# Kernel tuning notes

Hardware: AMD Instinct MI355X
Metric: run time of the kernel (lower is better)

The kernel has to match this reference:

```python
import jax, jax.numpy as jnp
import numpy as np

# Model dims
B, T, E, H = 2, 2048, 512, 8
HEAD_DIM = E // H            # 64
NUM_SCALES = 4               # Gauss-Laguerre quadrature nodes
NUM_PRF = 16                 # positive random features per scale
POLY_DIM = 16                # degree-2 TensorSketch dim
EPS = 1e-5
CHUNK = 128                  # chunk size for exact chunked causal linear attention


def setup_inputs() -> dict:
    key = jax.random.key(0)
    ks = jax.random.split(key, 10)
    x = jax.random.normal(ks[0], (B, T, E), jnp.float32)
    sc = 1.0 / np.sqrt(E)  # xavier-ish scale for square projections
    Wq = jax.random.normal(ks[1], (E, E), jnp.float32) * sc
    Wk = jax.random.normal(ks[2], (E, E), jnp.float32) * sc
    Wv = jax.random.normal(ks[3], (E, E), jnp.float32) * sc
    Wo = jax.random.normal(ks[4], (E, E), jnp.float32) * sc
    # FAVOR+ gaussian projections, one block per quadrature scale
    projections = jax.random.normal(ks[5], (NUM_SCALES, NUM_PRF, HEAD_DIM), jnp.float32)
    # Gauss-Laguerre nodes/weights for 1/(C - 2 q.k) = int_0^inf exp(-t(C - 2 q.k)) dt
    nodes, weights = np.polynomial.laguerre.laggauss(NUM_SCALES)
    coef = weights * np.exp(nodes) * np.exp(-nodes * EPS)
    scales = jnp.asarray(np.stack([nodes, coef], axis=1), jnp.float32)  # [S, 2] = (t_s, c_s)
    # degree-2 TensorSketch (count-sketch hashes + rademacher signs)
    sketch_h = jax.random.randint(ks[6], (2, HEAD_DIM), 0, POLY_DIM)
    sketch_s = (jax.random.randint(ks[7], (2, HEAD_DIM), 0, 2) * 2 - 1).astype(jnp.float32)
    return dict(x=x, Wq=Wq, Wk=Wk, Wv=Wv, Wo=Wo, projections=projections,
                scales=scales, sketch_h=sketch_h, sketch_s=sketch_s)


def _features(u, projections, scales, sketch_h, sketch_s):
    """Multi-scale FAVOR+ x TensorSketch feature map for the spherical YAT kernel.

    u: [B,T,H,d], unit-normalized along d. Returns [B,T,H, P*S*m].
    Phi(q).Phi(k) ~= (q.k)^2 / (||q-k||^2 + eps).
    """
    t = scales[:, 0]  # quadrature nodes t_s
    c = scales[:, 1]  # quadrature coeffs w_s e^{t_s} e^{-t_s eps}
    S, m, d = projections.shape
    z = jnp.einsum('smd,bthd->bthsm', projections, u)
    # exp(2 t q.k) via positive RFs; extra e^{-t||u||^2}=e^{-t} (unit sphere) folded in -> -2t
    ef = jnp.exp(jnp.sqrt(2.0 * t)[:, None] * z - 2.0 * t[:, None]) * jnp.sqrt(c / m)[:, None]  # [B,T,H,S,m]
    # degree-2 TensorSketch: countsketch via one-hot matmul, combine with FFT conv
    M1 = sketch_s[0][:, None] * jax.nn.one_hot(sketch_h[0], POLY_DIM, dtype=u.dtype)  # [d,P]
    M2 = sketch_s[1][:, None] * jax.nn.one_hot(sketch_h[1], POLY_DIM, dtype=u.dtype)
    ts = jnp.fft.irfft(jnp.fft.rfft(u @ M1) * jnp.fft.rfft(u @ M2), n=POLY_DIM)  # [B,T,H,P]
    Bs, Ts, Hs = u.shape[:3]
    ef = ef.reshape(Bs, Ts, Hs, S * m)
    return (ts[..., :, None] * ef[..., None, :]).reshape(Bs, Ts, Hs, POLY_DIM * S * m)


def reference(x, Wq, Wk, Wv, Wo, projections, scales, sketch_h, sketch_s):
    Bx, Tx, Ex = x.shape
    d = HEAD_DIM
    q = (x @ Wq).reshape(Bx, Tx, H, d)
    k = (x @ Wk).reshape(Bx, Tx, H, d)
    v = (x @ Wv).reshape(Bx, Tx, H, d)
    # spherical: project q,k to unit sphere
    qn = q / (jnp.linalg.norm(q, axis=-1, keepdims=True) + 1e-6)
    kn = k / (jnp.linalg.norm(k, axis=-1, keepdims=True) + 1e-6)
    fq = _features(qn, projections, scales, sketch_h, sketch_s)  # [B,T,H,F]
    fk = _features(kn, projections, scales, sketch_h, sketch_s)
    F = fq.shape[-1]
    # exact chunked causal linear attention: O(T) state, no [T,T] matrix
    N = Tx // CHUNK
    fq_ = fq.reshape(Bx, N, CHUNK, H, F)
    fk_ = fk.reshape(Bx, N, CHUNK, H, F)
    v_ = v.reshape(Bx, N, CHUNK, H, d)
    kv = jnp.einsum('bnchf,bnchd->bnhfd', fk_, v_)   # per-chunk sum of phi(k) v^T
    kz = fk_.sum(axis=2)                              # [B,N,H,F]
    kv_prev = jnp.concatenate([jnp.zeros_like(kv[:, :1]), jnp.cumsum(kv, axis=1)[:, :-1]], axis=1)
    kz_prev = jnp.concatenate([jnp.zeros_like(kz[:, :1]), jnp.cumsum(kz, axis=1)[:, :-1]], axis=1)
    num = jnp.einsum('bnchf,bnhfd->bnchd', fq_, kv_prev)
    den = jnp.einsum('bnchf,bnhf->bnch', fq_, kz_prev)
    # intra-chunk causal part
    sc = jnp.einsum('bnchf,bnkhf->bnhck', fq_, fk_)
    mask = jnp.tril(jnp.ones((CHUNK, CHUNK), bool))
    scm = jnp.where(mask, sc, 0.0)
    num = num + jnp.einsum('bnhck,bnkhd->bnchd', scm, v_)
    den = den + jnp.swapaxes(scm.sum(axis=-1), 2, 3)
    out = num / (den[..., None] + EPS)
    out = out.reshape(Bx, Tx, Ex) @ Wo
    return out
```

## Files before the change

### kernel.cpp

```cpp
#include <hip/hip_runtime.h>
#include <math.h>

#define B_ 2
#define T_ 2048
#define E_ 512
#define H_ 8
#define D_ 64
#define NCH 16
#define CH 128
#define EPS_ 1e-5f

__global__ __launch_bounds__(256) void gemm512(const float* __restrict__ A,
                                               const float* __restrict__ W,
                                               float* __restrict__ C) {
  __shared__ float As[16][68];
  __shared__ float Bs[16][68];
  const int tid = threadIdx.x;
  const int tx = tid & 15, ty = tid >> 4;
  const int row0 = blockIdx.x * 64, col0 = blockIdx.y * 64;
  const int lr = tid >> 2, lk = (tid & 3) * 4;
  const int bkr = tid >> 4, bcc = (tid & 15) * 4;
  float acc[4][4] = {};
  for (int k0 = 0; k0 < 512; k0 += 16) {
    float4 a4 = *(const float4*)(A + (size_t)(row0 + lr) * 512 + k0 + lk);
    As[lk + 0][lr] = a4.x; As[lk + 1][lr] = a4.y;
    As[lk + 2][lr] = a4.z; As[lk + 3][lr] = a4.w;
    *(float4*)&Bs[bkr][bcc] = *(const float4*)(W + (size_t)(k0 + bkr) * 512 + col0 + bcc);
    __syncthreads();
#pragma unroll
    for (int kk = 0; kk < 16; ++kk) {
      float4 av = *(const float4*)&As[kk][ty * 4];
      float4 bv = *(const float4*)&Bs[kk][tx * 4];
      float aa[4] = {av.x, av.y, av.z, av.w};
      float bb[4] = {bv.x, bv.y, bv.z, bv.w};
#pragma unroll
      for (int i = 0; i < 4; ++i)
#pragma unroll
        for (int j = 0; j < 4; ++j) acc[i][j] += aa[i] * bb[j];
    }
    __syncthreads();
  }
#pragma unroll
  for (int i = 0; i < 4; ++i) {
    float4 o = make_float4(acc[i][0], acc[i][1], acc[i][2], acc[i][3]);
    *(float4*)(C + (size_t)(row0 + ty * 4 + i) * 512 + col0 + tx * 4) = o;
  }
}

__global__ __launch_bounds__(128) void feat_kernel(
    const float* __restrict__ q, const float* __restrict__ k, const float* __restrict__ v,
    const float* __restrict__ proj, const float* __restrict__ scales,
    const int* __restrict__ sh, const float* __restrict__ ss,
    float* __restrict__ Tq, float* __restrict__ Eq,
    float* __restrict__ Tk, float* __restrict__ Ek, float* __restrict__ vh) {
  __shared__ float pj[64][64];
  __shared__ float sq2t[4], m2t[4], cf[4];
  __shared__ int h1[64], h2[64];
  __shared__ float s1[64], s2[64];
  const int tid = threadIdx.x;
  for (int i = tid; i < 4096; i += 128) pj[i >> 6][i & 63] = proj[i];
  if (tid < 4) {
    float t = scales[tid * 2], c = scales[tid * 2 + 1];
    sq2t[tid] = sqrtf(2.f * t); m2t[tid] = -2.f * t; cf[tid] = sqrtf(c / 16.f);
  }
  if (tid < 64) { h1[tid] = sh[tid]; h2[tid] = sh[64 + tid]; s1[tid] = ss[tid]; s2[tid] = ss[64 + tid]; }
  __syncthreads();
  const int isK = blockIdx.y;
  const int row = blockIdx.x * 128 + tid;
  const int h = row & 7; const int bt = row >> 3;
  const int t = bt & (T_ - 1); const int b = bt >> 11;
  const size_t src = (size_t)bt * 512 + h * 64;
  const size_t orow = (size_t)(b * H_ + h) * T_ + t;
  const float* in = (isK ? k : q) + src;
  float* To = (isK ? Tk : Tq) + orow * 16;
  float* Eo = (isK ? Ek : Eq) + orow * 64;

  float u[64]; float nrm = 0.f;
#pragma unroll
  for (int d = 0; d < 64; ++d) { float xv = in[d]; u[d] = xv; nrm += xv * xv; }
  const float inv = 1.f / (sqrtf(nrm) + 1e-6f);
#pragma unroll
  for (int d = 0; d < 64; ++d) u[d] *= inv;

  float p1[16], p2[16];
#pragma unroll
  for (int j = 0; j < 16; ++j) {
    float a1 = 0.f, a2 = 0.f;
#pragma unroll
    for (int d = 0; d < 64; ++d) {
      a1 += (h1[d] == j ? s1[d] : 0.f) * u[d];
      a2 += (h2[d] == j ? s2[d] : 0.f) * u[d];
    }
    p1[j] = a1; p2[j] = a2;
  }
  float tsv[16];
#pragma unroll
  for (int r = 0; r < 16; ++r) {
    float a = 0.f;
#pragma unroll
    for (int j = 0; j < 16; ++j) a += p1[j] * p2[(r - j) & 15];
    tsv[r] = a;
  }
#pragma unroll
  for (int p = 0; p < 16; ++p) To[p] = tsv[p];

#pragma unroll
  for (int s = 0; s < 4; ++s) {
    const float sq = sq2t[s], mb = m2t[s], c = cf[s];
#pragma unroll
    for (int m = 0; m < 16; ++m) {
      float z = 0.f;
      const float* pr = &pj[s * 16 + m][0];
#pragma unroll
      for (int d = 0; d < 64; ++d) z += pr[d] * u[d];
      Eo[s * 16 + m] = expf(sq * z + mb) * c;
    }
  }

  if (!isK) {
    const size_t bt0 = (size_t)blockIdx.x * 16;
    for (int i = tid; i < 16 * 512; i += 128) {
      const size_t bt2 = bt0 + (i >> 9);
      const int hh = (i >> 6) & 7, dd = i & 63;
      const int t2 = (int)(bt2 & (T_ - 1)); const int b2 = (int)(bt2 >> 11);
      vh[((size_t)(b2 * H_ + hh) * T_ + t2) * 64 + dd] = v[bt0 * 512 + i];
    }
  }
}

__global__ __launch_bounds__(256) void kv_kernel(const float* __restrict__ Tk, const float* __restrict__ Ek,
                                                 const float* __restrict__ vh, float* __restrict__ KV) {
  const int bhn = blockIdx.x;
  const int slice = blockIdx.y;
  __shared__ float tks[128][16];
  __shared__ float eks[128][16];
  __shared__ float vs[128][64];
  const int tid = threadIdx.x;
  const size_t rowbase = (size_t)bhn * 128;
  for (int i = tid; i < 2048; i += 256) tks[i >> 4][i & 15] = Tk[rowbase * 16 + i];
  for (int i = tid; i < 2048; i += 256) { int r = i >> 4, e = i & 15; eks[r][e] = Ek[(rowbase + r) * 64 + slice * 16 + e]; }
  for (int i = tid; i < 8192; i += 256) vs[i >> 6][i & 63] = vh[rowbase * 64 + i];
  __syncthreads();
  const int d = tid & 63, er = tid >> 6;
  float acc[4][16] = {};
  for (int c = 0; c < 128; ++c) {
    float tkc[16];
#pragma unroll
    for (int p = 0; p < 16; ++p) tkc[p] = tks[c][p];
    const float w = vs[c][d];
#pragma unroll
    for (int i = 0; i < 4; ++i) {
      const float a = eks[c][er * 4 + i] * w;
#pragma unroll
      for (int p = 0; p < 16; ++p) acc[i][p] += tkc[p] * a;
    }
  }
  float* out = KV + (size_t)bhn * 65536;
#pragma unroll
  for (int i = 0; i < 4; ++i)
#pragma unroll
    for (int p = 0; p < 16; ++p)
      out[(size_t)(p * 64 + slice * 16 + er * 4 + i) * 64 + d] = acc[i][p];
}

__global__ __launch_bounds__(256) void kz_kernel(const float* __restrict__ Tk, const float* __restrict__ Ek,
                                                 float* __restrict__ KZ) {
  const int bhn = blockIdx.x;
  __shared__ float tks[128][16];
  __shared__ float eks[128][64];
  const int tid = threadIdx.x;
  const size_t rowbase = (size_t)bhn * 128;
  for (int i = tid; i < 2048; i += 256) tks[i >> 4][i & 15] = Tk[rowbase * 16 + i];
  for (int i = tid; i < 8192; i += 256) eks[i >> 6][i & 63] = Ek[rowbase * 64 + i];
  __syncthreads();
  float acc[4] = {};
  for (int c = 0; c < 128; ++c) {
#pragma unroll
    for (int i = 0; i < 4; ++i) {
      const int item = tid + 256 * i;
      acc[i] += tks[c][item >> 6] * eks[c][item & 63];
    }
  }
#pragma unroll
  for (int i = 0; i < 4; ++i) KZ[(size_t)bhn * 1024 + tid + 256 * i] = acc[i];
}

__global__ void cumsum_kernel(float* __restrict__ KV, float* __restrict__ KZ) {
  const size_t idx = (size_t)blockIdx.x * 256 + threadIdx.x;
  const size_t nkv = (size_t)B_ * H_ * 65536;
  if (idx < nkv) {
    const size_t bh = idx >> 16, j = idx & 65535;
    float* p = KV + bh * NCH * 65536 + j;
    float a = 0.f;
#pragma unroll
    for (int n = 0; n < NCH; ++n) { const float t = p[(size_t)n << 16]; p[(size_t)n << 16] = a; a += t; }
  } else {
    const size_t i2 = idx - nkv;
    if (i2 < (size_t)B_ * H_ * 1024) {
      const size_t bh = i2 >> 10, j = i2 & 1023;
      float* p = KZ + bh * NCH * 1024 + j;
      float a = 0.f;
#pragma unroll
      for (int n = 0; n < NCH; ++n) { const float t = p[n << 10]; p[n << 10] = a; a += t; }
    }
  }
}

__global__ __launch_bounds__(256) void intra_kernel(const float* __restrict__ Tq, const float* __restrict__ Eq,
                                                    const float* __restrict__ Tk, const float* __restrict__ Ek,
                                                    const float* __restrict__ vh,
                                                    float* __restrict__ numb, float* __restrict__ den) {
  const int bhn = blockIdx.x;
  __shared__ float tks[64][16];
  __shared__ float eks[64][64];
  __shared__ float vs[64][64];
  const int tid = threadIdx.x;
  const int c = tid >> 1, half = tid & 1;
  const size_t rowbase = (size_t)bhn * 128;
  const size_t myrow = rowbase + c;
  float tq[16], eq[64];
#pragma unroll
  for (int p = 0; p < 16; ++p) tq[p] = Tq[myrow * 16 + p];
#pragma unroll
  for (int e = 0; e < 64; ++e) eq[e] = Eq[myrow * 64 + e];
  float num[32] = {};
  float dn = 0.f;
  for (int kh = 0; kh < 2; ++kh) {
    __syncthreads();
    for (int i = tid; i < 1024; i += 256) tks[i >> 4][i & 15] = Tk[(rowbase + kh * 64) * 16 + i];
    for (int i = tid; i < 4096; i += 256) eks[i >> 6][i & 63] = Ek[(rowbase + kh * 64) * 64 + i];
    for (int i = tid; i < 4096; i += 256) vs[i >> 6][i & 63] = vh[(rowbase + kh * 64) * 64 + i];
    __syncthreads();
    const int kmax = c - kh * 64;
    for (int kk = 0; kk < 64; ++kk) {
      if (kk > kmax) break;
      float dT = 0.f;
#pragma unroll
      for (int p = 0; p < 16; ++p) dT += tq[p] * tks[kk][p];
      float dE = 0.f;
#pragma unroll
      for (int e = 0; e < 64; ++e) dE += eq[e] * eks[kk][e];
      const float s = dT * dE;
      dn += s;
#pragma unroll
      for (int j = 0; j < 32; ++j) num[j] += s * vs[kk][half * 32 + j];
    }
  }
#pragma unroll
  for (int j = 0; j < 32; ++j) numb[myrow * 64 + half * 32 + j] = num[j];
  if (half == 0) den[myrow] = dn;
}

__global__ __launch_bounds__(256) void inter_kernel(const float* __restrict__ Tq, const float* __restrict__ Eq,
                                                    const float* __restrict__ KV, const float* __restrict__ KZ,
                                                    const float* __restrict__ numb, const float* __restrict__ den,
                                                    float* __restrict__ att) {
  const int bhn = blockIdx.x;
  const int n = bhn & 15, bh = bhn >> 4;
  const int b = bh >> 3, h = bh & 7;
  __shared__ float tqs[128][17];
  __shared__ float eqs[128][68];
  __shared__ float kvp[64][68];
  __shared__ float kzp[64];
  const int tid = threadIdx.x;
  const int tx = tid & 15, ty = tid >> 4;
  const size_t rowbase = (size_t)bhn * 128;
  for (int i = tid; i < 2048; i += 256) tqs[i >> 4][i & 15] = Tq[rowbase * 16 + i];
  for (int i = tid; i < 8192; i += 256) eqs[i >> 6][i & 63] = Eq[rowbase * 64 + i];
  float acc[8][4] = {};
  float accd[8] = {};
  const float* kvb = KV + (size_t)bhn * 65536;
  for (int p = 0; p < 16; ++p) {
    __syncthreads();
    for (int i = tid; i < 4096; i += 256) kvp[i >> 6][i & 63] = kvb[p * 4096 + i];
    if (tid < 64) kzp[tid] = KZ[(size_t)bhn * 1024 + p * 64 + tid];
    __syncthreads();
    float tqv[8];
#pragma unroll
    for (int ci = 0; ci < 8; ++ci) tqv[ci] = tqs[ty + 16 * ci][p];
    for (int e = 0; e < 64; ++e) {
      const float4 kv4 = *(const float4*)&kvp[e][tx * 4];
      const float kz = kzp[e];
#pragma unroll
      for (int ci = 0; ci < 8; ++ci) {
        const float a = tqv[ci] * eqs[ty + 16 * ci][e];
        acc[ci][0] += a * kv4.x; acc[ci][1] += a * kv4.y;
        acc[ci][2] += a * kv4.z; acc[ci][3] += a * kv4.w;
        accd[ci] += a * kz;
      }
    }
  }
#pragma unroll
  for (int ci = 0; ci < 8; ++ci) {
    const int cc = ty + 16 * ci;
    const size_t row = rowbase + cc;
    const int t = n * 128 + cc;
    const float invd = 1.f / (den[row] + accd[ci] + EPS_);
    float4 o;
    o.x = (numb[row * 64 + tx * 4 + 0] + acc[ci][0]) * invd;
    o.y = (numb[row * 64 + tx * 4 + 1] + acc[ci][1]) * invd;
    o.z = (numb[row * 64 + tx * 4 + 2] + acc[ci][2]) * invd;
    o.w = (numb[row * 64 + tx * 4 + 3] + acc[ci][3]) * invd;
    *(float4*)(att + (size_t)(b * T_ + t) * 512 + h * 64 + tx * 4) = o;
  }
}

extern "C" void kernel_launch(void* const* d_in, const int* in_sizes, int n_in,
                              void* d_out, int out_size, void* d_ws, size_t ws_size,
                              hipStream_t stream) {
  const float* x   = (const float*)d_in[0];
  const float* Wq  = (const float*)d_in[1];
  const float* Wk  = (const float*)d_in[2];
  const float* Wv  = (const float*)d_in[3];
  const float* Wo  = (const float*)d_in[4];
  const float* prj = (const float*)d_in[5];
  const float* scl = (const float*)d_in[6];
  const int*   shh = (const int*)d_in[7];
  const float* sss = (const float*)d_in[8];

  float* ws  = (float*)d_ws;
  float* q   = ws;
  float* k   = q + 2097152;
  float* v   = k + 2097152;
  float* Tq  = v + 2097152;
  float* Eq  = Tq + 524288;
  float* Tk  = Eq + 2097152;
  float* Ek  = Tk + 524288;
  float* vh  = Ek + 2097152;
  float* KV  = vh + 2097152;
  float* KZ  = KV + 16777216;
  float* nmb = KZ + 262144;
  float* den = nmb + 2097152;
  float* att = den + 32768;

  dim3 gg(64, 8);
  hipLaunchKernelGGL(gemm512, gg, dim3(256), 0, stream, x, Wq, q);
  hipLaunchKernelGGL(gemm512, gg, dim3(256), 0, stream, x, Wk, k);
  hipLaunchKernelGGL(gemm512, gg, dim3(256), 0, stream, x, Wv, v);
  hipLaunchKernelGGL(feat_kernel, dim3(256, 2), dim3(128), 0, stream,
                     q, k, v, prj, scl, shh, sss, Tq, Eq, Tk, Ek, vh);
  hipLaunchKernelGGL(kv_kernel, dim3(256, 4), dim3(256), 0, stream, Tk, Ek, vh, KV);
  hipLaunchKernelGGL(kz_kernel, dim3(256), dim3(256), 0, stream, Tk, Ek, KZ);
  hipLaunchKernelGGL(cumsum_kernel, dim3(4160), dim3(256), 0, stream, KV, KZ);
  hipLaunchKernelGGL(intra_kernel, dim3(256), dim3(256), 0, stream, Tq, Eq, Tk, Ek, vh, nmb, den);
  hipLaunchKernelGGL(inter_kernel, dim3(256), dim3(256), 0, stream, Tq, Eq, KV, KZ, nmb, den, att);
  hipLaunchKernelGGL(gemm512, gg, dim3(256), 0, stream, att, Wo, (float*)d_out);
}
```

Measured before the change: 502.5 us.

## Split intra/inter attention kernels across row halves and vectorize shared-memory accesses

Gives the intra- and inter-chunk kernels a second grid dimension, so each block handles 64 query rows instead of 128. This doubles the block count and lowers per-thread register pressure. The intra kernel also loads all needed keys into shared memory at once, so it has no inner barriers. Shared-memory reads in the kv, kz, intra and inter kernels become float4 loads, with padded rows to ease bank conflicts. In exchange, shared-memory use in intra grows and each half-block reloads KV.

```diff
diff --git a/kernel.cpp b/kernel.cpp
--- a/kernel.cpp
+++ b/kernel.cpp
@@ -132,28 +132,34 @@
                                                  const float* __restrict__ vh, float* __restrict__ KV) {
   const int bhn = blockIdx.x;
   const int slice = blockIdx.y;
-  __shared__ float tks[128][16];
+  __shared__ float tks[128][20];
   __shared__ float eks[128][16];
   __shared__ float vs[128][64];
   const int tid = threadIdx.x;
   const size_t rowbase = (size_t)bhn * 128;
   for (int i = tid; i < 2048; i += 256) tks[i >> 4][i & 15] = Tk[rowbase * 16 + i];
   for (int i = tid; i < 2048; i += 256) { int r = i >> 4, e = i & 15; eks[r][e] = Ek[(rowbase + r) * 64 + slice * 16 + e]; }
-  for (int i = tid; i < 8192; i += 256) vs[i >> 6][i & 63] = vh[rowbase * 64 + i];
+  for (int i = tid; i < 2048; i += 256) {
+    float4 v4 = *(const float4*)(vh + rowbase * 64 + 4 * i);
+    *(float4*)&vs[(4 * i) >> 6][(4 * i) & 63] = v4;
+  }
   __syncthreads();
   const int d = tid & 63, er = tid >> 6;
   float acc[4][16] = {};
   for (int c = 0; c < 128; ++c) {
-    float tkc[16];
-#pragma unroll
-    for (int p = 0; p < 16; ++p) tkc[p] = tks[c][p];
+    float4 t0 = *(const float4*)&tks[c][0];
+    float4 t1 = *(const float4*)&tks[c][4];
+    float4 t2 = *(const float4*)&tks[c][8];
+    float4 t3 = *(const float4*)&tks[c][12];
+    float tkc[16] = {t0.x, t0.y, t0.z, t0.w, t1.x, t1.y, t1.z, t1.w,
+                     t2.x, t2.y, t2.z, t2.w, t3.x, t3.y, t3.z, t3.w};
+    float4 e4 = *(const float4*)&eks[c][er * 4];
     const float w = vs[c][d];
-#pragma unroll
-    for (int i = 0; i < 4; ++i) {
-      const float a = eks[c][er * 4 + i] * w;
-#pragma unroll
-      for (int p = 0; p < 16; ++p) acc[i][p] += tkc[p] * a;
-    }
+    float ai[4] = {e4.x * w, e4.y * w, e4.z * w, e4.w * w};
+#pragma unroll
+    for (int i = 0; i < 4; ++i)
+#pragma unroll
+      for (int p = 0; p < 16; ++p) acc[i][p] += tkc[p] * ai[i];
   }
   float* out = KV + (size_t)bhn * 65536;
 #pragma unroll
@@ -166,23 +172,25 @@
 __global__ __launch_bounds__(256) void kz_kernel(const float* __restrict__ Tk, const float* __restrict__ Ek,
                                                  float* __restrict__ KZ) {
   const int bhn = blockIdx.x;
-  __shared__ float tks[128][16];
+  __shared__ float tks[128][20];
   __shared__ float eks[128][64];
   const int tid = threadIdx.x;
   const size_t rowbase = (size_t)bhn * 128;
   for (int i = tid; i < 2048; i += 256) tks[i >> 4][i & 15] = Tk[rowbase * 16 + i];
-  for (int i = tid; i < 8192; i += 256) eks[i >> 6][i & 63] = Ek[rowbase * 64 + i];
+  for (int i = tid; i < 2048; i += 256) {
+    float4 v4 = *(const float4*)(Ek + rowbase * 64 + 4 * i);
+    *(float4*)&eks[(4 * i) >> 6][(4 * i) & 63] = v4;
+  }
   __syncthreads();
-  float acc[4] = {};
+  const int e = tid & 63, p0 = (tid >> 6) * 4;
+  float a[4] = {};
   for (int c = 0; c < 128; ++c) {
-#pragma unroll
-    for (int i = 0; i < 4; ++i) {
-      const int item = tid + 256 * i;
-      acc[i] += tks[c][item >> 6] * eks[c][item & 63];
-    }
-  }
-#pragma unroll
-  for (int i = 0; i < 4; ++i) KZ[(size_t)bhn * 1024 + tid + 256 * i] = acc[i];
+    float4 t4 = *(const float4*)&tks[c][p0];
+    const float ek = eks[c][e];
+    a[0] += t4.x * ek; a[1] += t4.y * ek; a[2] += t4.z * ek; a[3] += t4.w * ek;
+  }
+#pragma unroll
+  for (int j = 0; j < 4; ++j) KZ[(size_t)bhn * 1024 + (p0 + j) * 64 + e] = a[j];
 }
 
 __global__ void cumsum_kernel(float* __restrict__ KV, float* __restrict__ KZ) {
@@ -211,44 +219,66 @@
                                                     const float* __restrict__ vh,
                                                     float* __restrict__ numb, float* __restrict__ den) {
   const int bhn = blockIdx.x;
-  __shared__ float tks[64][16];
-  __shared__ float eks[64][64];
-  __shared__ float vs[64][64];
-  const int tid = threadIdx.x;
-  const int c = tid >> 1, half = tid & 1;
-  const size_t rowbase = (size_t)bhn * 128;
-  const size_t myrow = rowbase + c;
+  const int rh = blockIdx.y;
+  __shared__ float tks[128][20];
+  __shared__ float eks[128][68];
+  __shared__ float vs[128][68];
+  const int tid = threadIdx.x;
+  const int r = tid >> 2, dg = tid & 3, d0 = dg * 16;
+  const int nk = (rh + 1) * 64;
+  const size_t chunkbase = (size_t)bhn * 128;
+  const size_t myrow = chunkbase + rh * 64 + r;
+
+  for (int i = tid; i < nk * 16; i += 256) tks[i >> 4][i & 15] = Tk[chunkbase * 16 + i];
+  for (int i = tid; i < nk * 16; i += 256) {
+    float4 e4 = *(const float4*)(Ek + chunkbase * 64 + 4 * i);
+    *(float4*)&eks[(4 * i) >> 6][(4 * i) & 63] = e4;
+    float4 w4 = *(const float4*)(vh + chunkbase * 64 + 4 * i);
+    *(float4*)&vs[(4 * i) >> 6][(4 * i) & 63] = w4;
+  }
   float tq[16], eq[64];
 #pragma unroll
-  for (int p = 0; p < 16; ++p) tq[p] = Tq[myrow * 16 + p];
-#pragma unroll
-  for (int e = 0; e < 64; ++e) eq[e] = Eq[myrow * 64 + e];
-  float num[32] = {};
+  for (int pp = 0; pp < 4; ++pp) {
+    float4 t4 = *(const float4*)(Tq + myrow * 16 + pp * 4);
+    tq[pp * 4 + 0] = t4.x; tq[pp * 4 + 1] = t4.y; tq[pp * 4 + 2] = t4.z; tq[pp * 4 + 3] = t4.w;
+  }
+#pragma unroll
+  for (int ee = 0; ee < 16; ++ee) {
+    float4 e4 = *(const float4*)(Eq + myrow * 64 + ee * 4);
+    eq[ee * 4 + 0] = e4.x; eq[ee * 4 + 1] = e4.y; eq[ee * 4 + 2] = e4.z; eq[ee * 4 + 3] = e4.w;
+  }
+  __syncthreads();
+
+  float num[16] = {};
   float dn = 0.f;
-  for (int kh = 0; kh < 2; ++kh) {
-    __syncthreads();
-    for (int i = tid; i < 1024; i += 256) tks[i >> 4][i & 15] = Tk[(rowbase + kh * 64) * 16 + i];
-    for (int i = tid; i < 4096; i += 256) eks[i >> 6][i & 63] = Ek[(rowbase + kh * 64) * 64 + i];
-    for (int i = tid; i < 4096; i += 256) vs[i >> 6][i & 63] = vh[(rowbase + kh * 64) * 64 + i];
-    __syncthreads();
-    const int kmax = c - kh * 64;
-    for (int kk = 0; kk < 64; ++kk) {
-      if (kk > kmax) break;
-      float dT = 0.f;
-#pragma unroll
-      for (int p = 0; p < 16; ++p) dT += tq[p] * tks[kk][p];
-      float dE = 0.f;
-#pragma unroll
-      for (int e = 0; e < 64; ++e) dE += eq[e] * eks[kk][e];
-      const float s = dT * dE;
-      dn += s;
-#pragma unroll
-      for (int j = 0; j < 32; ++j) num[j] += s * vs[kk][half * 32 + j];
-    }
-  }
-#pragma unroll
-  for (int j = 0; j < 32; ++j) numb[myrow * 64 + half * 32 + j] = num[j];
-  if (half == 0) den[myrow] = dn;
+  const int kmax = rh * 64 + r;
+  for (int kk = 0; kk <= kmax; ++kk) {
+    float dT = 0.f, dE = 0.f;
+#pragma unroll
+    for (int pp = 0; pp < 4; ++pp) {
+      float4 t4 = *(const float4*)&tks[kk][pp * 4];
+      dT += tq[pp * 4 + 0] * t4.x + tq[pp * 4 + 1] * t4.y + tq[pp * 4 + 2] * t4.z + tq[pp * 4 + 3] * t4.w;
+    }
+#pragma unroll
+    for (int ee = 0; ee < 16; ++ee) {
+      float4 e4 = *(const float4*)&eks[kk][ee * 4];
+      dE += eq[ee * 4 + 0] * e4.x + eq[ee * 4 + 1] * e4.y + eq[ee * 4 + 2] * e4.z + eq[ee * 4 + 3] * e4.w;
+    }
+    const float s = dT * dE;
+    dn += s;
+#pragma unroll
+    for (int jj = 0; jj < 4; ++jj) {
+      float4 v4 = *(const float4*)&vs[kk][d0 + jj * 4];
+      num[jj * 4 + 0] += s * v4.x; num[jj * 4 + 1] += s * v4.y;
+      num[jj * 4 + 2] += s * v4.z; num[jj * 4 + 3] += s * v4.w;
+    }
+  }
+#pragma unroll
+  for (int jj = 0; jj < 4; ++jj) {
+    float4 o = make_float4(num[jj * 4 + 0], num[jj * 4 + 1], num[jj * 4 + 2], num[jj * 4 + 3]);
+    *(float4*)(numb + myrow * 64 + d0 + jj * 4) = o;
+  }
+  if (dg == 0) den[myrow] = dn;
 }
 
 __global__ __launch_bounds__(256) void inter_kernel(const float* __restrict__ Tq, const float* __restrict__ Eq,
@@ -256,51 +286,69 @@
                                                     const float* __restrict__ numb, const float* __restrict__ den,
                                                     float* __restrict__ att) {
   const int bhn = blockIdx.x;
+  const int rh = blockIdx.y;
   const int n = bhn & 15, bh = bhn >> 4;
   const int b = bh >> 3, h = bh & 7;
-  __shared__ float tqs[128][17];
-  __shared__ float eqs[128][68];
+  __shared__ float tqs[64][17];
+  __shared__ float eqs[64][68];
   __shared__ float kvp[64][68];
   __shared__ float kzp[64];
   const int tid = threadIdx.x;
   const int tx = tid & 15, ty = tid >> 4;
-  const size_t rowbase = (size_t)bhn * 128;
-  for (int i = tid; i < 2048; i += 256) tqs[i >> 4][i & 15] = Tq[rowbase * 16 + i];
-  for (int i = tid; i < 8192; i += 256) eqs[i >> 6][i & 63] = Eq[rowbase * 64 + i];
-  float acc[8][4] = {};
-  float accd[8] = {};
+  const size_t rowbase = (size_t)bhn * 128 + rh * 64;
+  for (int i = tid; i < 1024; i += 256) tqs[i >> 4][i & 15] = Tq[rowbase * 16 + i];
+  for (int i = tid; i < 1024; i += 256) {
+    float4 v4 = *(const float4*)(Eq + rowbase * 64 + 4 * i);
+    *(float4*)&eqs[i >> 4][(i & 15) * 4] = v4;
+  }
   const float* kvb = KV + (size_t)bhn * 65536;
+  const float* kzb = KZ + (size_t)bhn * 1024;
+  float acc[4][4] = {};
+  float accd[4] = {};
   for (int p = 0; p < 16; ++p) {
     __syncthreads();
-    for (int i = tid; i < 4096; i += 256) kvp[i >> 6][i & 63] = kvb[p * 4096 + i];
-    if (tid < 64) kzp[tid] = KZ[(size_t)bhn * 1024 + p * 64 + tid];
+#pragma unroll
+    for (int j = 0; j < 4; ++j) {
+      const int f = tid + 256 * j;
+      float4 v4 = *(const float4*)(kvb + p * 4096 + 4 * f);
+      *(float4*)&kvp[f >> 4][(f & 15) * 4] = v4;
+    }
+    if (tid < 64) kzp[tid] = kzb[p * 64 + tid];
     __syncthreads();
-    float tqv[8];
-#pragma unroll
-    for (int ci = 0; ci < 8; ++ci) tqv[ci] = tqs[ty + 16 * ci][p];
-    for (int e = 0; e < 64; ++e) {
-      const float4 kv4 = *(const float4*)&kvp[e][tx * 4];
-      const float kz = kzp[e];
-#pragma unroll
-      for (int ci = 0; ci < 8; ++ci) {
-        const float a = tqv[ci] * eqs[ty + 16 * ci][e];
-        acc[ci][0] += a * kv4.x; acc[ci][1] += a * kv4.y;
-        acc[ci][2] += a * kv4.z; acc[ci][3] += a * kv4.w;
-        accd[ci] += a * kz;
+    float tqv[4];
+#pragma unroll
+    for (int ci = 0; ci < 4; ++ci) tqv[ci] = tqs[ty + 16 * ci][p];
+    for (int e0 = 0; e0 < 64; e0 += 4) {
+      float4 kz4 = *(const float4*)&kzp[e0];
+      float4 kv0 = *(const float4*)&kvp[e0 + 0][tx * 4];
+      float4 kv1 = *(const float4*)&kvp[e0 + 1][tx * 4];
+      float4 kv2 = *(const float4*)&kvp[e0 + 2][tx * 4];
+      float4 kv3 = *(const float4*)&kvp[e0 + 3][tx * 4];
+#pragma unroll
+      for (int ci = 0; ci < 4; ++ci) {
+        float4 eq4 = *(const float4*)&eqs[ty + 16 * ci][e0];
+        const float a0 = tqv[ci] * eq4.x, a1 = tqv[ci] * eq4.y;
+        const float a2 = tqv[ci] * eq4.z, a3 = tqv[ci] * eq4.w;
+        acc[ci][0] += a0 * kv0.x; acc[ci][1] += a0 * kv0.y; acc[ci][2] += a0 * kv0.z; acc[ci][3] += a0 * kv0.w;
+        acc[ci][0] += a1 * kv1.x; acc[ci][1] += a1 * kv1.y; acc[ci][2] += a1 * kv1.z; acc[ci][3] += a1 * kv1.w;
+        acc[ci][0] += a2 * kv2.x; acc[ci][1] += a2 * kv2.y; acc[ci][2] += a2 * kv2.z; acc[ci][3] += a2 * kv2.w;
+        acc[ci][0] += a3 * kv3.x; acc[ci][1] += a3 * kv3.y; acc[ci][2] += a3 * kv3.z; acc[ci][3] += a3 * kv3.w;
+        accd[ci] += a0 * kz4.x + a1 * kz4.y + a2 * kz4.z + a3 * kz4.w;
       }
     }
   }
 #pragma unroll
-  for (int ci = 0; ci < 8; ++ci) {
-    const int cc = ty + 16 * ci;
-    const size_t row = rowbase + cc;
-    const int t = n * 128 + cc;
+  for (int ci = 0; ci < 4; ++ci) {
+    const int rloc = ty + 16 * ci;
+    const size_t row = rowbase + rloc;
+    const int t = n * 128 + rh * 64 + rloc;
     const float invd = 1.f / (den[row] + accd[ci] + EPS_);
+    float4 nm = *(const float4*)(numb + row * 64 + tx * 4);
     float4 o;
-    o.x = (numb[row * 64 + tx * 4 + 0] + acc[ci][0]) * invd;
-    o.y = (numb[row * 64 + tx * 4 + 1] + acc[ci][1]) * invd;
-    o.z = (numb[row * 64 + tx * 4 + 2] + acc[ci][2]) * invd;
-    o.w = (numb[row * 64 + tx * 4 + 3] + acc[ci][3]) * invd;
+    o.x = (nm.x + acc[ci][0]) * invd;
+    o.y = (nm.y + acc[ci][1]) * invd;
+    o.z = (nm.z + acc[ci][2]) * invd;
+    o.w = (nm.w + acc[ci][3]) * invd;
     *(float4*)(att + (size_t)(b * T_ + t) * 512 + h * 64 + tx * 4) = o;
   }
 }
@@ -342,7 +390,7 @@
   hipLaunchKernelGGL(kv_kernel, dim3(256, 4), dim3(256), 0, stream, Tk, Ek, vh, KV);
   hipLaunchKernelGGL(kz_kernel, dim3(256), dim3(256), 0, stream, Tk, Ek, KZ);
   hipLaunchKernelGGL(cumsum_kernel, dim3(4160), dim3(256), 0, stream, KV, KZ);
-  hipLaunchKernelGGL(intra_kernel, dim3(256), dim3(256), 0, stream, Tq, Eq, Tk, Ek, vh, nmb, den);
-  hipLaunchKernelGGL(inter_kernel, dim3(256), dim3(256), 0, stream, Tq, Eq, KV, KZ, nmb, den, att);
+  hipLaunchKernelGGL(intra_kernel, dim3(256, 2), dim3(256), 0, stream, Tq, Eq, Tk, Ek, vh, nmb, den);
+  hipLaunchKernelGGL(inter_kernel, dim3(256, 2), dim3(256), 0, stream, Tq, Eq, KV, KZ, nmb, den, att);
   hipLaunchKernelGGL(gemm512, gg, dim3(256), 0, stream, att, Wo, (float*)d_out);
 }
```

Result: faster. 481.0 us (-4.3%).
